# Optimization experiments

Hardware: AMD Instinct MI355X
Metric: run time of the kernel (lower is better)

The kernel has to match this reference:

```python
import jax, jax.numpy as jnp
import numpy as np

DIM = 128
H = 8
NEG_SLOPE = 0.2
SCALE = 12.0
N_ITEMS = 81920
E_INT = 163840
N_T = 4096
NUM_NODE = 40000


def _normalize(x, eps=1e-12):
    n = jnp.linalg.norm(x, axis=-1, keepdims=True)
    return x / jnp.maximum(n, eps)


def _gat(feat, src, dst, fc_w, attn_l, attn_r, bias):
    # GATConv with residual (Identity, since in_feats == out_feats) and bias.
    N = feat.shape[0]
    fs = (feat @ fc_w.T).reshape(N, H, DIM)                # [N,H,D]
    el = jnp.einsum('nhd,hd->nh', fs, attn_l)              # [N,H]
    er = jnp.einsum('nhd,hd->nh', fs, attn_r)              # [N,H]
    e = el[src] + er[dst]                                  # u_add_v -> [E,H]
    e = jnp.where(e >= 0, e, NEG_SLOPE * e)                # leaky_relu
    # edge_softmax grouped by destination node
    emax = jax.ops.segment_max(e, dst, num_segments=N)
    ex = jnp.exp(e - emax[dst])
    denom = jax.ops.segment_sum(ex, dst, num_segments=N)
    a = ex / denom[dst]                                    # [E,H]
    # u_mul_e + sum aggregation
    m = fs[src] * a[:, :, None]                            # [E,H,D]
    rst = jax.ops.segment_sum(m, dst, num_segments=N)      # [N,H,D]
    rst = rst + feat[:, None, :] + bias.reshape(1, H, DIM)
    return rst


def setup_inputs() -> dict:
    key = jax.random.key(0)
    ks = jax.random.split(key, 20)
    stdv = 1.0 / np.sqrt(DIM)

    def unif(k, shape):
        return jax.random.uniform(k, shape, jnp.float32, -stdv, stdv)

    return {
        'iid': jax.random.randint(ks[0], (N_ITEMS,), 0, NUM_NODE),
        'tid': jax.random.randint(ks[1], (N_T,), 0, 10),
        'pid': jax.random.randint(ks[2], (N_ITEMS,), 0, 200),
        'src_i': jax.random.randint(ks[3], (E_INT,), 0, N_ITEMS),
        'dst_i': jax.random.randint(ks[4], (E_INT,), 0, N_ITEMS),
        'agg_src': jnp.arange(N_ITEMS),
        'agg_dst': jnp.sort(jax.random.randint(ks[5], (N_ITEMS,), 0, N_T)),
        'last_nodes': jax.random.randint(ks[6], (N_T,), 0, N_ITEMS),
        'emb': unif(ks[7], (NUM_NODE, DIM)),
        'pos_emb': unif(ks[8], (200, DIM)),
        'target_emb': unif(ks[9], (10, DIM)),
        'gat1_fc': unif(ks[10], (H * DIM, DIM)),
        'gat1_al': unif(ks[11], (H, DIM)),
        'gat1_ar': unif(ks[12], (H, DIM)),
        'gat1_b': jnp.zeros((H * DIM,), jnp.float32),
        'gat2_fc': unif(ks[13], (H * DIM, DIM)),
        'gat2_al': unif(ks[14], (H, DIM)),
        'gat2_ar': unif(ks[15], (H, DIM)),
        'gat2_b': jnp.zeros((H * DIM,), jnp.float32),
        'q_w': unif(ks[16], (DIM, 2 * DIM)),
        'fc_sr_w': unif(ks[17], (DIM, 2 * DIM)),
    }


def reference(iid, tid, pid, src_i, dst_i, agg_src, agg_dst, last_nodes,
              emb, pos_emb, target_emb,
              gat1_fc, gat1_al, gat1_ar, gat1_b,
              gat2_fc, gat2_al, gat2_ar, gat2_b,
              q_w, fc_sr_w):
    h_v = _normalize(emb[iid])                              # [N_items, D]
    h_p = pos_emb[pid]                                      # [E_agg, D]
    h_t = target_emb[tid]                                   # [N_T, D]

    # gat1 on interacts; gat2 on reversed interacts; max over heads each
    h1 = _gat(h_v, src_i, dst_i, gat1_fc, gat1_al, gat1_ar, gat1_b).max(axis=1)
    h2 = _gat(h_v, dst_i, src_i, gat2_fc, gat2_al, gat2_ar, gat2_b).max(axis=1)
    h = _normalize(h1 + h2)                                 # [N_items, D]

    # PosAggregator over 'agg' edges (item -> target)
    ft = h[agg_src]                                         # [E_agg, D]
    e = jnp.tanh(jnp.concatenate([ft, h_p], axis=-1) @ q_w.T)
    w = jnp.sum(e * h_t[agg_dst], axis=-1, keepdims=True)   # udf_agg weight
    sr_g = jax.ops.segment_sum(ft * w, agg_dst, num_segments=h_t.shape[0])
    sr_l = h[last_nodes]                                    # last-item features

    sr = jnp.concatenate([sr_g, sr_l], axis=-1) @ fc_sr_w.T
    scores = SCALE * (_normalize(sr) @ _normalize(emb).T)   # [N_T, num_node]
    return scores
```

## Files before the change

### kernel.cpp

```cpp
#include <hip/hip_runtime.h>
#include <stdint.h>

#define DD 128
#define HN 8
#define NITEMS 81920
#define EINT 163840
#define NT 4096
#define NV 40000
#define NVPAD 40064
#define EAGG 81920
#define NEG_SLOPE 0.2f
#define SCALE 12.0f

typedef unsigned short u16;
typedef __attribute__((ext_vector_type(8))) short bf16x8;
typedef __attribute__((ext_vector_type(4))) float f32x4;
typedef __attribute__((ext_vector_type(4))) unsigned short u16x4;

__device__ __forceinline__ float bf2f(unsigned short u){ return __uint_as_float(((unsigned)u)<<16); }
__device__ __forceinline__ unsigned short f2bf(float f){
  unsigned u = __float_as_uint(f);
  u += 0x7fffu + ((u>>16)&1u);
  return (unsigned short)(u>>16);
}

__global__ __launch_bounds__(256) void k_cast3(const float* __restrict__ fc1, const float* __restrict__ fc2,
    const float* __restrict__ qw, const float* __restrict__ fcsr,
    u16* __restrict__ w1, u16* __restrict__ w2, u16* __restrict__ qb, float* __restrict__ fT){
  int i = blockIdx.x*256 + threadIdx.x;
  if (i < 131072) w1[i] = f2bf(fc1[i]);
  else if (i < 262144) w2[i-131072] = f2bf(fc2[i-131072]);
  else if (i < 294912) qb[i-262144] = f2bf(qw[i-262144]);
  else if (i < 327680){
    int j = i - 294912;
    int k = j >> 7, col = j & 127;
    fT[j] = fcsr[(size_t)col*256 + k];
  }
}

__global__ __launch_bounds__(128) void k_prep_u(const float* __restrict__ fc1, const float* __restrict__ al1,
    const float* __restrict__ ar1, const float* __restrict__ fc2, const float* __restrict__ al2,
    const float* __restrict__ ar2, u16* __restrict__ U){
  int r = blockIdx.x, k = threadIdx.x;
  if (r >= 32){ U[(size_t)r*DD + k] = 0; return; }
  int g = r>>3, h = r&7;
  const float* fc = (g>=2)? fc2 : fc1;
  const float* av = (g==0)? al1 : (g==1)? ar1 : (g==2)? al2 : ar2;
  float s = 0.f;
  for (int d=0; d<DD; ++d) s += fc[(size_t)(h*DD+d)*DD + k] * av[h*DD+d];
  U[(size_t)r*DD + k] = f2bf(s);
}

__global__ __launch_bounds__(256) void k_norm(const float* __restrict__ emb, const int* __restrict__ iid,
    u16* __restrict__ nemb, u16* __restrict__ hvb, int* __restrict__ cnt){
  int gi = blockIdx.x*256 + threadIdx.x;
  if (gi < 2*NITEMS) cnt[gi] = 0;
  int w = gi >> 6;
  int lane = gi & 63;
  u16* dst; const float* src;
  if (w < NVPAD){
    dst = nemb + (size_t)w*DD;
    if (w >= NV){ dst[lane*2]=0; dst[lane*2+1]=0; return; }
    src = emb + (size_t)w*DD;
  } else {
    int n = w - NVPAD;
    dst = hvb + (size_t)n*DD;
    src = emb + (size_t)iid[n]*DD;
  }
  float2 v = *(const float2*)(src + lane*2);
  float ss = v.x*v.x + v.y*v.y;
  #pragma unroll
  for (int m=1;m<64;m<<=1) ss += __shfl_xor(ss, m);
  float inv = 1.f / fmaxf(sqrtf(ss), 1e-12f);
  dst[lane*2]   = f2bf(v.x*inv);
  dst[lane*2+1] = f2bf(v.y*inv);
}

template<int OUT_BF16>
__global__ __launch_bounds__(256) void gemm_nt(const u16* __restrict__ A, const u16* __restrict__ B,
                                               void* __restrict__ C, int M, int N, int K,
                                               float alpha, int ldc, int nvalid){
  __shared__ u16 As[128*32];
  __shared__ u16 Bs[128*32];
  int m0 = blockIdx.x*128, n0 = blockIdx.y*128;
  int t = threadIdx.x, lane = t&63, wid = t>>6;
  int wm = wid>>1, wn = wid&1;
  f32x4 zero = {0.f,0.f,0.f,0.f};
  f32x4 acc[4][4];
  #pragma unroll
  for (int i=0;i<4;i++)
    #pragma unroll
    for (int j=0;j<4;j++) acc[i][j] = zero;
  int lr = lane & 15, lk = (lane>>4)*8;
  for (int k0=0; k0<K; k0+=32){
    #pragma unroll
    for (int cc=0; cc<2; ++cc){
      int c = t + cc*256;
      int row = c>>2, col = (c&3)*8;
      *(bf16x8*)(void*)&As[c*8] = *(const bf16x8*)(const void*)&A[(size_t)(m0+row)*K + k0 + col];
      *(bf16x8*)(void*)&Bs[c*8] = *(const bf16x8*)(const void*)&B[(size_t)(n0+row)*K + k0 + col];
    }
    __syncthreads();
    bf16x8 af[4], bfr[4];
    #pragma unroll
    for (int m=0;m<4;m++) af[m]  = *(const bf16x8*)(const void*)&As[(wm*64+m*16+lr)*32 + lk];
    #pragma unroll
    for (int n=0;n<4;n++) bfr[n] = *(const bf16x8*)(const void*)&Bs[(wn*64+n*16+lr)*32 + lk];
    #pragma unroll
    for (int m=0;m<4;m++)
      #pragma unroll
      for (int n=0;n<4;n++)
        acc[m][n] = __builtin_amdgcn_mfma_f32_16x16x32_bf16(af[m], bfr[n], acc[m][n], 0,0,0);
    __syncthreads();
  }
  #pragma unroll
  for (int m=0;m<4;m++)
    #pragma unroll
    for (int n=0;n<4;n++)
      #pragma unroll
      for (int r=0;r<4;r++){
        int row = m0 + wm*64 + m*16 + (lane>>4)*4 + r;
        int col = n0 + wn*64 + n*16 + (lane&15);
        if (col < nvalid){
          float v = acc[m][n][r]*alpha;
          if (OUT_BF16) ((u16*)C)[(size_t)row*ldc + col] = f2bf(v);
          else          ((float*)C)[(size_t)row*ldc + col] = v;
        }
      }
}

__global__ __launch_bounds__(256) void k_deg2(const int* __restrict__ di, const int* __restrict__ si,
                                              int* __restrict__ cnt){
  int i = blockIdx.x*256+threadIdx.x;
  if (i<EINT){ atomicAdd(&cnt[di[i]],1); atomicAdd(&cnt[NITEMS+si[i]],1); }
}

__global__ __launch_bounds__(256) void k_scan_a(int* cnt, int* off, int* bsum, int n){
  __shared__ int buf[256];
  int b = blockIdx.x, t = threadIdx.x, i = b*256+t;
  int v = (i<n)? cnt[i] : 0;
  buf[t] = v; __syncthreads();
  #pragma unroll
  for (int ofs=1; ofs<256; ofs<<=1){
    int x = (t>=ofs)? buf[t-ofs] : 0;
    __syncthreads();
    buf[t] += x;
    __syncthreads();
  }
  if (i<n){ off[i] = buf[t]-v; cnt[i] = 0; }
  if (t==255) bsum[b] = buf[255];
}

__global__ __launch_bounds__(1024) void k_scan_b(int* bsum, int* off, int nb, int n){
  __shared__ int buf[1024];
  int t = threadIdx.x;
  int v = (t<nb)? bsum[t] : 0;
  buf[t]=v; __syncthreads();
  #pragma unroll
  for (int ofs=1; ofs<1024; ofs<<=1){
    int x=(t>=ofs)?buf[t-ofs]:0; __syncthreads(); buf[t]+=x; __syncthreads();
  }
  if (t<nb) bsum[t] = buf[t]-v;
  if (t==1023) off[n] = buf[1023];
}

__global__ __launch_bounds__(256) void k_scan_c(int* __restrict__ off, const int* __restrict__ bsum, int n){
  int i = blockIdx.x*256+threadIdx.x;
  if (i<n) off[i] += bsum[blockIdx.x];
}

__global__ __launch_bounds__(256) void k_scatter2(const int* __restrict__ di, const int* __restrict__ si,
    const int* __restrict__ off, int* __restrict__ cnt, int* __restrict__ sid){
  int i = blockIdx.x*256+threadIdx.x;
  if (i<EINT){
    int a = di[i];         sid[off[a]+atomicAdd(&cnt[a],1)] = si[i];
    int b = NITEMS+si[i];  sid[off[b]+atomicAdd(&cnt[b],1)] = di[i];
  }
}

__global__ __launch_bounds__(256) void k_aw(const int* __restrict__ off, const int* __restrict__ sid,
    const float* __restrict__ ecat, u16* __restrict__ aw){
  int u = blockIdx.x*256 + threadIdx.x;
  if (u >= 2*NITEMS) return;
  int g = (u >= NITEMS) ? 1 : 0;
  int w = u - g*NITEMS;
  int cl = g*16, cr = g*16 + 8;
  float ern[8];
  #pragma unroll
  for (int h=0;h<8;h++) ern[h] = ecat[(size_t)w*32 + cr + h];
  int lo = off[u], hi = off[u+1];
  float den[8];
  #pragma unroll
  for (int h=0;h<8;h++) den[h] = 0.f;
  for (int i=lo;i<hi;++i){
    const float* e = ecat + (size_t)sid[i]*32 + cl;
    #pragma unroll
    for (int h=0;h<8;h++){
      float lv = e[h] + ern[h];
      lv = (lv>=0.f)? lv : NEG_SLOPE*lv;
      den[h] += expf(lv);
    }
  }
  float inv[8];
  #pragma unroll
  for (int h=0;h<8;h++) inv[h] = (den[h]>0.f)? 1.f/den[h] : 0.f;
  for (int i=lo;i<hi;++i){
    const float* e = ecat + (size_t)sid[i]*32 + cl;
    bf16x8 o;
    #pragma unroll
    for (int h=0;h<8;h++){
      float lv = e[h] + ern[h];
      lv = (lv>=0.f)? lv : NEG_SLOPE*lv;
      o[h] = (short)f2bf(expf(lv)*inv[h]);
    }
    *(bf16x8*)(void*)&aw[(size_t)i*8] = o;
  }
}

__global__ __launch_bounds__(256) void k_agg(const int* __restrict__ off, const int* __restrict__ sid,
    const u16* __restrict__ aw, const u16* __restrict__ hvb, u16* __restrict__ agg, int obase){
  int w = (blockIdx.x*256 + threadIdx.x) >> 6;
  int lane = threadIdx.x & 63;
  if (w >= NITEMS) return;
  int lo = off[obase+w], hi = off[obase+w+1];
  float a0[8], a1[8];
  #pragma unroll
  for (int h=0;h<8;h++){ a0[h]=0.f; a1[h]=0.f; }
  for (int i=lo; i<hi; ++i){
    int s = sid[i];
    unsigned v = *(const unsigned*)(const void*)&hvb[(size_t)s*DD + lane*2];
    float f0 = bf2f((u16)(v & 0xffffu)), f1 = bf2f((u16)(v >> 16));
    bf16x8 w8 = *(const bf16x8*)(const void*)&aw[(size_t)i*8];
    #pragma unroll
    for (int h=0;h<8;h++){
      float wa = bf2f((u16)w8[h]);
      a0[h] += wa*f0; a1[h] += wa*f1;
    }
  }
  #pragma unroll
  for (int h=0;h<8;h++){
    unsigned o = (unsigned)f2bf(a0[h]) | ((unsigned)f2bf(a1[h])<<16);
    *(unsigned*)(void*)&agg[(size_t)w*1024 + h*DD + lane*2] = o;
  }
}

template<int MODE>
__global__ __launch_bounds__(512) void k_hg(const u16* __restrict__ agg, const u16* __restrict__ wfc,
    const float* __restrict__ bias, const u16* __restrict__ hvb,
    u16* __restrict__ h1b, u16* __restrict__ hb){
  __shared__ __align__(16) char smem[52224];
  u16* As = (u16*)smem;
  u16* Bs = As + 64*136;
  float* F = (float*)smem;
  int n0 = blockIdx.x*64;
  int t = threadIdx.x, lane = t&63, wid = t>>6;
  int wm = wid&3, wn = wid>>2;
  int lr = lane&15, lq = lane>>4;
  int ar = t>>3, ak = (t&7)*16;
  f32x4 rm[4];
  #pragma unroll
  for (int n=0;n<4;n++){ f32x4 z={-1e30f,-1e30f,-1e30f,-1e30f}; rm[n]=z; }
  for (int h=0; h<HN; ++h){
    *(bf16x8*)(void*)&As[ar*136 + ak]     = *(const bf16x8*)(const void*)&agg[(size_t)(n0+ar)*1024 + h*DD + ak];
    *(bf16x8*)(void*)&As[ar*136 + ak + 8] = *(const bf16x8*)(const void*)&agg[(size_t)(n0+ar)*1024 + h*DD + ak + 8];
    #pragma unroll
    for (int cc=0; cc<2; ++cc){
      int c = t + cc*512;
      int br = c>>3, bk = (c&7)*16;
      *(bf16x8*)(void*)&Bs[br*136 + bk]     = *(const bf16x8*)(const void*)&wfc[(size_t)(h*DD+br)*DD + bk];
      *(bf16x8*)(void*)&Bs[br*136 + bk + 8] = *(const bf16x8*)(const void*)&wfc[(size_t)(h*DD+br)*DD + bk + 8];
    }
    __syncthreads();
    f32x4 acc[4];
    #pragma unroll
    for (int n=0;n<4;n++){ f32x4 z={0.f,0.f,0.f,0.f}; acc[n]=z; }
    #pragma unroll
    for (int ks=0; ks<4; ++ks){
      bf16x8 af = *(const bf16x8*)(const void*)&As[(wm*16+lr)*136 + ks*32 + lq*8];
      #pragma unroll
      for (int n=0;n<4;n++){
        bf16x8 bfr = *(const bf16x8*)(const void*)&Bs[(wn*64+n*16+lr)*136 + ks*32 + lq*8];
        acc[n] = __builtin_amdgcn_mfma_f32_16x16x32_bf16(af, bfr, acc[n], 0,0,0);
      }
    }
    #pragma unroll
    for (int n=0;n<4;n++){
      float bn = bias[h*DD + wn*64 + n*16 + lr];
      #pragma unroll
      for (int r=0;r<4;r++) rm[n][r] = fmaxf(rm[n][r], acc[n][r] + bn);
    }
    __syncthreads();
  }
  if (MODE==0){
    #pragma unroll
    for (int n=0;n<4;n++)
      #pragma unroll
      for (int r=0;r<4;r++){
        int row = n0 + wm*16 + lq*4 + r;
        int col = wn*64 + n*16 + lr;
        h1b[(size_t)row*DD + col] = f2bf(rm[n][r] + bf2f(hvb[(size_t)row*DD + col]));
      }
  } else {
    #pragma unroll
    for (int n=0;n<4;n++)
      #pragma unroll
      for (int r=0;r<4;r++){
        int lrow = wm*16 + lq*4 + r;
        int col = wn*64 + n*16 + lr;
        int row = n0 + lrow;
        F[lrow*DD + col] = rm[n][r] + bf2f(hvb[(size_t)row*DD + col]) + bf2f(h1b[(size_t)row*DD + col]);
      }
    __syncthreads();
    int r8 = t>>3, q = t&7;
    float vals[16];
    float ss = 0.f;
    #pragma unroll
    for (int j=0;j<16;j++){ vals[j] = F[r8*DD + q*16 + j]; ss += vals[j]*vals[j]; }
    ss += __shfl_xor(ss,1); ss += __shfl_xor(ss,2); ss += __shfl_xor(ss,4);
    float inv = 1.f/fmaxf(sqrtf(ss),1e-12f);
    bf16x8 o0, o1;
    #pragma unroll
    for (int j=0;j<8;j++){ o0[j] = (short)f2bf(vals[j]*inv); o1[j] = (short)f2bf(vals[8+j]*inv); }
    *(bf16x8*)(void*)&hb[(size_t)(n0+r8)*DD + q*16]     = o0;
    *(bf16x8*)(void*)&hb[(size_t)(n0+r8)*DD + q*16 + 8] = o1;
  }
}

__global__ __launch_bounds__(256) void k_epw(const int* __restrict__ asrc, const int* __restrict__ pid,
    const int* __restrict__ adst, const int* __restrict__ tid_, const u16* __restrict__ hb,
    const float* __restrict__ pemb, const u16* __restrict__ qwb, const float* __restrict__ temb,
    float* __restrict__ wv){
  __shared__ u16 As[128*32];
  __shared__ u16 Bs[128*32];
  __shared__ float tembS[10*DD];
  __shared__ float wsum[128];
  __shared__ int rowtt[128];
  int m0 = blockIdx.x*128;
  int t = threadIdx.x, lane = t&63, wid = t>>6;
  int wm = wid>>1, wn = wid&1, lr = lane&15, lq = lane>>4;
  for (int i=t; i<10*DD; i+=256) tembS[i] = temb[i];
  if (t < 128){ rowtt[t] = tid_[adst[m0+t]]; wsum[t] = 0.f; }
  f32x4 zero = {0.f,0.f,0.f,0.f};
  f32x4 acc[4][4];
  #pragma unroll
  for (int i=0;i<4;i++)
    #pragma unroll
    for (int j=0;j<4;j++) acc[i][j] = zero;
  for (int k0=0; k0<256; k0+=32){
    #pragma unroll
    for (int cc=0; cc<2; ++cc){
      int c = t + cc*256;
      int row = c>>2;
      int kk = k0 + (c&3)*8;
      bf16x8 av;
      if (k0 < 128){
        av = *(const bf16x8*)(const void*)&hb[(size_t)asrc[m0+row]*DD + kk];
      } else {
        const float* p = pemb + (size_t)pid[m0+row]*DD + (kk-128);
        float4 p0 = *(const float4*)p;
        float4 p1 = *(const float4*)(p+4);
        av[0]=(short)f2bf(p0.x); av[1]=(short)f2bf(p0.y); av[2]=(short)f2bf(p0.z); av[3]=(short)f2bf(p0.w);
        av[4]=(short)f2bf(p1.x); av[5]=(short)f2bf(p1.y); av[6]=(short)f2bf(p1.z); av[7]=(short)f2bf(p1.w);
      }
      *(bf16x8*)(void*)&As[c*8] = av;
      *(bf16x8*)(void*)&Bs[c*8] = *(const bf16x8*)(const void*)&qwb[(size_t)row*256 + kk];
    }
    __syncthreads();
    bf16x8 af[4], bfr[4];
    #pragma unroll
    for (int m=0;m<4;m++) af[m]  = *(const bf16x8*)(const void*)&As[(wm*64+m*16+lr)*32 + lq*8];
    #pragma unroll
    for (int n=0;n<4;n++) bfr[n] = *(const bf16x8*)(const void*)&Bs[(wn*64+n*16+lr)*32 + lq*8];
    #pragma unroll
    for (int m=0;m<4;m++)
      #pragma unroll
      for (int n=0;n<4;n++)
        acc[m][n] = __builtin_amdgcn_mfma_f32_16x16x32_bf16(af[m], bfr[n], acc[m][n], 0,0,0);
    __syncthreads();
  }
  #pragma unroll
  for (int m=0;m<4;m++)
    #pragma unroll
    for (int r=0;r<4;r++){
      int lrow = wm*64 + m*16 + lq*4 + r;
      int tt = rowtt[lrow];
      float p = 0.f;
      #pragma unroll
      for (int n=0;n<4;n++){
        int col = wn*64 + n*16 + lr;
        p += tanhf(acc[m][n][r]) * tembS[tt*DD + col];
      }
      #pragma unroll
      for (int msk=1; msk<16; msk<<=1) p += __shfl_xor(p, msk);
      if (lr==0) atomicAdd(&wsum[lrow], p);
    }
  __syncthreads();
  if (t < 128) wv[m0+t] = wsum[t];
}

__device__ __forceinline__ int lbound(const int* a, int n, int key){
  int lo=0, hi=n;
  while (lo<hi){ int mid=(lo+hi)>>1; if (a[mid]<key) lo=mid+1; else hi=mid; }
  return lo;
}

__global__ __launch_bounds__(256) void k_sr(const u16* __restrict__ hb, const float* __restrict__ w,
    const int* __restrict__ asrc, const int* __restrict__ adst, const int* __restrict__ lastn,
    const float* __restrict__ fcsrT, u16* __restrict__ nsr){
  __shared__ float cat[256];
  __shared__ float red[128];
  __shared__ int lohi[2];
  int t = blockIdx.x, tid = threadIdx.x;
  if (tid == 0){ lohi[0] = lbound(adst, EAGG, t); lohi[1] = lbound(adst, EAGG, t+1); }
  __syncthreads();
  int lo = lohi[0], hi = lohi[1];
  if (tid < DD){
    float a = 0.f;
    for (int i=lo;i<hi;++i) a += bf2f(hb[(size_t)asrc[i]*DD + tid]) * w[i];
    cat[tid] = a;
  } else {
    int d = tid - DD;
    cat[DD + d] = bf2f(hb[(size_t)lastn[t]*DD + d]);
  }
  __syncthreads();
  float s = 0.f;
  if (tid < DD){
    #pragma unroll 8
    for (int k=0;k<256;++k) s += cat[k]*fcsrT[(size_t)k*DD + tid];
    red[tid] = s*s;
  }
  __syncthreads();
  for (int st=64; st>0; st>>=1){
    if (tid < st) red[tid] += red[tid+st];
    __syncthreads();
  }
  if (tid < DD){
    float inv = 1.f/fmaxf(sqrtf(red[0]),1e-12f);
    nsr[(size_t)t*DD + tid] = f2bf(s*inv);
  }
}

__global__ __launch_bounds__(256) void gemm_sc(const u16* __restrict__ A, const u16* __restrict__ B,
                                               float* __restrict__ C){
  __shared__ __align__(16) char smem[16896];
  u16* As = (u16*)smem;
  u16* Bs = As + 4096;
  float* tr = (float*)smem;
  int flat = blockIdx.y*gridDim.x + blockIdx.x;
  int nf = (flat&7)*1252 + (flat>>3);
  int m0 = (nf & 31)*128;
  int n0 = (nf >> 5)*128;
  int t = threadIdx.x, lane = t&63, wid = t>>6;
  int wm = wid>>1, wn = wid&1, lr = lane&15, lq = lane>>4;
  f32x4 zero = {0.f,0.f,0.f,0.f};
  f32x4 acc[4][4];
  #pragma unroll
  for (int i=0;i<4;i++)
    #pragma unroll
    for (int j=0;j<4;j++) acc[i][j] = zero;
  for (int k0=0; k0<DD; k0+=32){
    #pragma unroll
    for (int cc=0; cc<2; ++cc){
      int c = t + cc*256;
      int row = c>>2, col = (c&3)*8;
      *(bf16x8*)(void*)&As[c*8] = *(const bf16x8*)(const void*)&A[(size_t)(m0+row)*DD + k0 + col];
      *(bf16x8*)(void*)&Bs[c*8] = *(const bf16x8*)(const void*)&B[(size_t)(n0+row)*DD + k0 + col];
    }
    __syncthreads();
    bf16x8 af[4], bfr[4];
    #pragma unroll
    for (int m=0;m<4;m++) af[m]  = *(const bf16x8*)(const void*)&As[(wm*64+m*16+lr)*32 + lq*8];
    #pragma unroll
    for (int n=0;n<4;n++) bfr[n] = *(const bf16x8*)(const void*)&Bs[(wn*64+n*16+lr)*32 + lq*8];
    #pragma unroll
    for (int m=0;m<4;m++)
      #pragma unroll
      for (int n=0;n<4;n++)
        acc[m][n] = __builtin_amdgcn_mfma_f32_16x16x32_bf16(af[m], bfr[n], acc[m][n], 0,0,0);
    __syncthreads();
  }
  int rr = lane>>4;
  int cq = lane&15;
  #pragma unroll
  for (int m=0;m<4;m++){
    #pragma unroll
    for (int n=0;n<4;n++)
      #pragma unroll
      for (int r=0;r<4;r++)
        tr[wid*1040 + (lq*4+r)*65 + n*16 + lr] = acc[m][n][r]*SCALE;
    __syncthreads();
    #pragma unroll
    for (int rg=0; rg<4; ++rg){
      int row = rg*4 + rr;
      int grow = m0 + wm*64 + m*16 + row;
      int gcol = n0 + wn*64 + cq*4;
      if (gcol < NV)
        *(float4*)&C[(size_t)grow*NV + gcol] = *(const float4*)&tr[wid*1040 + row*65 + cq*4];
    }
    __syncthreads();
  }
}

extern "C" void kernel_launch(void* const* d_in, const int* in_sizes, int n_in,
                              void* d_out, int out_size, void* d_ws, size_t ws_size,
                              hipStream_t stream){
  (void)in_sizes; (void)n_in; (void)out_size; (void)ws_size;
  const int*   iid   = (const int*)d_in[0];
  const int*   tid_  = (const int*)d_in[1];
  const int*   pid   = (const int*)d_in[2];
  const int*   src_i = (const int*)d_in[3];
  const int*   dst_i = (const int*)d_in[4];
  const int*   asrc  = (const int*)d_in[5];
  const int*   adst  = (const int*)d_in[6];
  const int*   lastn = (const int*)d_in[7];
  const float* emb   = (const float*)d_in[8];
  const float* pemb  = (const float*)d_in[9];
  const float* temb  = (const float*)d_in[10];
  const float* fc1   = (const float*)d_in[11];
  const float* al1   = (const float*)d_in[12];
  const float* ar1   = (const float*)d_in[13];
  const float* b1    = (const float*)d_in[14];
  const float* fc2   = (const float*)d_in[15];
  const float* al2   = (const float*)d_in[16];
  const float* ar2   = (const float*)d_in[17];
  const float* b2    = (const float*)d_in[18];
  const float* qw    = (const float*)d_in[19];
  const float* fcsr  = (const float*)d_in[20];

  char* ws = (char*)d_ws;
  size_t o = 0;
  auto alc = [&](size_t b)->char*{ char* r = ws + o; o += (b + 511) & ~(size_t)511; return r; };
  u16*   hvb  = (u16*)  alc((size_t)NITEMS*DD*2);
  u16*   hb   = (u16*)  alc((size_t)NITEMS*DD*2);
  u16*   h1b  = (u16*)  alc((size_t)NITEMS*DD*2);
  float* ecat = (float*)alc((size_t)NITEMS*32*4);
  int*   off  = (int*)  alc((size_t)(2*NITEMS+1)*4);
  int*   cnt  = (int*)  alc((size_t)(2*NITEMS)*4);
  int*   bsum = (int*)  alc((size_t)1024*4);
  int*   sid  = (int*)  alc((size_t)(2*EINT)*4);
  u16*   aw   = (u16*)  alc((size_t)(2*EINT)*8*2);
  u16*   wfc1 = (u16*)  alc((size_t)1024*DD*2);
  u16*   wfc2 = (u16*)  alc((size_t)1024*DD*2);
  u16*   qwb  = (u16*)  alc((size_t)DD*256*2);
  float* fT   = (float*)alc((size_t)256*DD*4);
  u16*   Umat = (u16*)  alc((size_t)128*DD*2);
  float* wv   = (float*)alc((size_t)EAGG*4);
  u16*   nsr  = (u16*)  alc((size_t)NT*DD*2);
  u16*   nemb = (u16*)  alc((size_t)NVPAD*DD*2);
  u16*   agg  = (u16*)  alc((size_t)NITEMS*1024*2);

  const int N2 = 2*NITEMS;
  const int NB2 = N2/256;

  k_norm<<<(NVPAD+NITEMS)/4, 256, 0, stream>>>(emb, iid, nemb, hvb, cnt);
  k_prep_u<<<128, 128, 0, stream>>>(fc1, al1, ar1, fc2, al2, ar2, Umat);
  k_cast3<<<1280, 256, 0, stream>>>(fc1, fc2, qw, fcsr, wfc1, wfc2, qwb, fT);
  gemm_nt<0><<<dim3(NITEMS/128, 1), 256, 0, stream>>>(hvb, Umat, ecat, NITEMS, 128, DD, 1.f, 32, 32);

  k_deg2<<<(EINT+255)/256, 256, 0, stream>>>(dst_i, src_i, cnt);
  k_scan_a<<<NB2, 256, 0, stream>>>(cnt, off, bsum, N2);
  k_scan_b<<<1, 1024, 0, stream>>>(bsum, off, NB2, N2);
  k_scan_c<<<NB2, 256, 0, stream>>>(off, bsum, N2);
  k_scatter2<<<(EINT+255)/256, 256, 0, stream>>>(dst_i, src_i, off, cnt, sid);

  k_aw<<<N2/256, 256, 0, stream>>>(off, sid, ecat, aw);

  k_agg<<<NITEMS/4, 256, 0, stream>>>(off, sid, aw, hvb, agg, 0);
  k_hg<0><<<NITEMS/64, 512, 0, stream>>>(agg, wfc1, b1, hvb, h1b, nullptr);
  k_agg<<<NITEMS/4, 256, 0, stream>>>(off, sid, aw, hvb, agg, NITEMS);
  k_hg<1><<<NITEMS/64, 512, 0, stream>>>(agg, wfc2, b2, hvb, h1b, hb);

  k_epw<<<EAGG/128, 256, 0, stream>>>(asrc, pid, adst, tid_, hb, pemb, qwb, temb, wv);
  k_sr<<<NT, 256, 0, stream>>>(hb, wv, asrc, adst, lastn, fT, nsr);

  gemm_sc<<<dim3(32, NVPAD/128), 256, 0, stream>>>(nsr, nemb, (float*)d_out);
}
```

Measured before the change: 554.6 us.

## Merge prep kernels, fold scan fixup into consumers, retile score GEMM

The three setup kernels (normalize, attention-vector projection, weight casts) become one launch with block ranges. The final scan-add kernel is removed: consumers add the per-block sum when they read offsets, and the scan writes a zero sentinel for the last block. The score GEMM moves to 64x256 tiles with a K step of 64, padded LDS rows and a 1D swizzled grid, with NVPAD raised to a multiple of 256. This cuts launch overhead and aims for better reuse and stores in the dominant output GEMM, at the cost of extra offset reads and more LDS per block.

```diff
diff --git a/kernel.cpp b/kernel.cpp
--- a/kernel.cpp
+++ b/kernel.cpp
@@ -7,10 +7,14 @@
 #define EINT 163840
 #define NT 4096
 #define NV 40000
-#define NVPAD 40064
+#define NVPAD 40192
 #define EAGG 81920
 #define NEG_SLOPE 0.2f
 #define SCALE 12.0f
+
+#define NB_NORM ((NVPAD + NITEMS)/4)
+#define NB_PU 64
+#define NB_CAST 1280
 
 typedef unsigned short u16;
 typedef __attribute__((ext_vector_type(8))) short bf16x8;
@@ -24,56 +28,56 @@
   return (unsigned short)(u>>16);
 }
 
-__global__ __launch_bounds__(256) void k_cast3(const float* __restrict__ fc1, const float* __restrict__ fc2,
+__global__ __launch_bounds__(256) void k_prep(const float* __restrict__ emb, const int* __restrict__ iid,
+    const float* __restrict__ fc1, const float* __restrict__ al1, const float* __restrict__ ar1,
+    const float* __restrict__ fc2, const float* __restrict__ al2, const float* __restrict__ ar2,
     const float* __restrict__ qw, const float* __restrict__ fcsr,
+    u16* __restrict__ nemb, u16* __restrict__ hvb, int* __restrict__ cnt, u16* __restrict__ U,
     u16* __restrict__ w1, u16* __restrict__ w2, u16* __restrict__ qb, float* __restrict__ fT){
-  int i = blockIdx.x*256 + threadIdx.x;
-  if (i < 131072) w1[i] = f2bf(fc1[i]);
-  else if (i < 262144) w2[i-131072] = f2bf(fc2[i-131072]);
-  else if (i < 294912) qb[i-262144] = f2bf(qw[i-262144]);
-  else if (i < 327680){
-    int j = i - 294912;
-    int k = j >> 7, col = j & 127;
-    fT[j] = fcsr[(size_t)col*256 + k];
-  }
-}
-
-__global__ __launch_bounds__(128) void k_prep_u(const float* __restrict__ fc1, const float* __restrict__ al1,
-    const float* __restrict__ ar1, const float* __restrict__ fc2, const float* __restrict__ al2,
-    const float* __restrict__ ar2, u16* __restrict__ U){
-  int r = blockIdx.x, k = threadIdx.x;
-  if (r >= 32){ U[(size_t)r*DD + k] = 0; return; }
-  int g = r>>3, h = r&7;
-  const float* fc = (g>=2)? fc2 : fc1;
-  const float* av = (g==0)? al1 : (g==1)? ar1 : (g==2)? al2 : ar2;
-  float s = 0.f;
-  for (int d=0; d<DD; ++d) s += fc[(size_t)(h*DD+d)*DD + k] * av[h*DD+d];
-  U[(size_t)r*DD + k] = f2bf(s);
-}
-
-__global__ __launch_bounds__(256) void k_norm(const float* __restrict__ emb, const int* __restrict__ iid,
-    u16* __restrict__ nemb, u16* __restrict__ hvb, int* __restrict__ cnt){
-  int gi = blockIdx.x*256 + threadIdx.x;
-  if (gi < 2*NITEMS) cnt[gi] = 0;
-  int w = gi >> 6;
-  int lane = gi & 63;
-  u16* dst; const float* src;
-  if (w < NVPAD){
-    dst = nemb + (size_t)w*DD;
-    if (w >= NV){ dst[lane*2]=0; dst[lane*2+1]=0; return; }
-    src = emb + (size_t)w*DD;
+  int b = blockIdx.x;
+  if (b < NB_NORM){
+    int gi = b*256 + threadIdx.x;
+    if (gi < 2*NITEMS) cnt[gi] = 0;
+    int w = gi >> 6;
+    int lane = gi & 63;
+    u16* dst; const float* src;
+    if (w < NVPAD){
+      dst = nemb + (size_t)w*DD;
+      if (w >= NV){ dst[lane*2]=0; dst[lane*2+1]=0; return; }
+      src = emb + (size_t)w*DD;
+    } else {
+      int n = w - NVPAD;
+      dst = hvb + (size_t)n*DD;
+      src = emb + (size_t)iid[n]*DD;
+    }
+    float2 v = *(const float2*)(src + lane*2);
+    float ss = v.x*v.x + v.y*v.y;
+    #pragma unroll
+    for (int m=1;m<64;m<<=1) ss += __shfl_xor(ss, m);
+    float inv = 1.f / fmaxf(sqrtf(ss), 1e-12f);
+    dst[lane*2]   = f2bf(v.x*inv);
+    dst[lane*2+1] = f2bf(v.y*inv);
+  } else if (b < NB_NORM + NB_PU){
+    int r = (b - NB_NORM)*2 + (threadIdx.x>>7);
+    int k = threadIdx.x & 127;
+    if (r >= 32){ U[(size_t)r*DD + k] = 0; return; }
+    int g = r>>3, h = r&7;
+    const float* fc = (g>=2)? fc2 : fc1;
+    const float* av = (g==0)? al1 : (g==1)? ar1 : (g==2)? al2 : ar2;
+    float s = 0.f;
+    for (int d=0; d<DD; ++d) s += fc[(size_t)(h*DD+d)*DD + k] * av[h*DD+d];
+    U[(size_t)r*DD + k] = f2bf(s);
   } else {
-    int n = w - NVPAD;
-    dst = hvb + (size_t)n*DD;
-    src = emb + (size_t)iid[n]*DD;
-  }
-  float2 v = *(const float2*)(src + lane*2);
-  float ss = v.x*v.x + v.y*v.y;
-  #pragma unroll
-  for (int m=1;m<64;m<<=1) ss += __shfl_xor(ss, m);
-  float inv = 1.f / fmaxf(sqrtf(ss), 1e-12f);
-  dst[lane*2]   = f2bf(v.x*inv);
-  dst[lane*2+1] = f2bf(v.y*inv);
+    int i = (b - NB_NORM - NB_PU)*256 + threadIdx.x;
+    if (i < 131072) w1[i] = f2bf(fc1[i]);
+    else if (i < 262144) w2[i-131072] = f2bf(fc2[i-131072]);
+    else if (i < 294912) qb[i-262144] = f2bf(qw[i-262144]);
+    else if (i < 327680){
+      int j = i - 294912;
+      int k = j >> 7, col = j & 127;
+      fT[j] = fcsr[(size_t)col*256 + k];
+    }
+  }
 }
 
 template<int OUT_BF16>
@@ -161,25 +165,21 @@
     int x=(t>=ofs)?buf[t-ofs]:0; __syncthreads(); buf[t]+=x; __syncthreads();
   }
   if (t<nb) bsum[t] = buf[t]-v;
+  else if (t==nb) bsum[t] = 0;
   if (t==1023) off[n] = buf[1023];
 }
 
-__global__ __launch_bounds__(256) void k_scan_c(int* __restrict__ off, const int* __restrict__ bsum, int n){
-  int i = blockIdx.x*256+threadIdx.x;
-  if (i<n) off[i] += bsum[blockIdx.x];
-}
-
 __global__ __launch_bounds__(256) void k_scatter2(const int* __restrict__ di, const int* __restrict__ si,
-    const int* __restrict__ off, int* __restrict__ cnt, int* __restrict__ sid){
+    const int* __restrict__ off, const int* __restrict__ bsum, int* __restrict__ cnt, int* __restrict__ sid){
   int i = blockIdx.x*256+threadIdx.x;
   if (i<EINT){
-    int a = di[i];         sid[off[a]+atomicAdd(&cnt[a],1)] = si[i];
-    int b = NITEMS+si[i];  sid[off[b]+atomicAdd(&cnt[b],1)] = di[i];
-  }
-}
-
-__global__ __launch_bounds__(256) void k_aw(const int* __restrict__ off, const int* __restrict__ sid,
-    const float* __restrict__ ecat, u16* __restrict__ aw){
+    int a = di[i];         sid[off[a]+bsum[a>>8]+atomicAdd(&cnt[a],1)] = si[i];
+    int b = NITEMS+si[i];  sid[off[b]+bsum[b>>8]+atomicAdd(&cnt[b],1)] = di[i];
+  }
+}
+
+__global__ __launch_bounds__(256) void k_aw(const int* __restrict__ off, const int* __restrict__ bsum,
+    const int* __restrict__ sid, const float* __restrict__ ecat, u16* __restrict__ aw){
   int u = blockIdx.x*256 + threadIdx.x;
   if (u >= 2*NITEMS) return;
   int g = (u >= NITEMS) ? 1 : 0;
@@ -188,7 +188,8 @@
   float ern[8];
   #pragma unroll
   for (int h=0;h<8;h++) ern[h] = ecat[(size_t)w*32 + cr + h];
-  int lo = off[u], hi = off[u+1];
+  int lo = off[u] + bsum[u>>8];
+  int hi = off[u+1] + bsum[(u+1)>>8];
   float den[8];
   #pragma unroll
   for (int h=0;h<8;h++) den[h] = 0.f;
@@ -217,12 +218,15 @@
   }
 }
 
-__global__ __launch_bounds__(256) void k_agg(const int* __restrict__ off, const int* __restrict__ sid,
-    const u16* __restrict__ aw, const u16* __restrict__ hvb, u16* __restrict__ agg, int obase){
+__global__ __launch_bounds__(256) void k_agg(const int* __restrict__ off, const int* __restrict__ bsum,
+    const int* __restrict__ sid, const u16* __restrict__ aw, const u16* __restrict__ hvb,
+    u16* __restrict__ agg, int obase){
   int w = (blockIdx.x*256 + threadIdx.x) >> 6;
   int lane = threadIdx.x & 63;
   if (w >= NITEMS) return;
-  int lo = off[obase+w], hi = off[obase+w+1];
+  int u = obase + w;
+  int lo = off[u] + bsum[u>>8];
+  int hi = off[u+1] + bsum[(u+1)>>8];
   float a0[8], a1[8];
   #pragma unroll
   for (int h=0;h<8;h++){ a0[h]=0.f; a1[h]=0.f; }
@@ -442,45 +446,52 @@
 
 __global__ __launch_bounds__(256) void gemm_sc(const u16* __restrict__ A, const u16* __restrict__ B,
                                                float* __restrict__ C){
-  __shared__ __align__(16) char smem[16896];
+  __shared__ __align__(16) char smem[46080];
   u16* As = (u16*)smem;
-  u16* Bs = As + 4096;
+  u16* Bs = As + 64*72;
   float* tr = (float*)smem;
-  int flat = blockIdx.y*gridDim.x + blockIdx.x;
-  int nf = (flat&7)*1252 + (flat>>3);
-  int m0 = (nf & 31)*128;
-  int n0 = (nf >> 5)*128;
+  int flat = blockIdx.x;
+  int nf = (flat&7)*1256 + (flat>>3);
+  int nti = nf % 157, mti = nf / 157;
+  int m0 = mti*64, n0 = nti*256;
   int t = threadIdx.x, lane = t&63, wid = t>>6;
-  int wm = wid>>1, wn = wid&1, lr = lane&15, lq = lane>>4;
+  int lr = lane&15, lq = lane>>4;
   f32x4 zero = {0.f,0.f,0.f,0.f};
   f32x4 acc[4][4];
   #pragma unroll
   for (int i=0;i<4;i++)
     #pragma unroll
     for (int j=0;j<4;j++) acc[i][j] = zero;
-  for (int k0=0; k0<DD; k0+=32){
-    #pragma unroll
-    for (int cc=0; cc<2; ++cc){
-      int c = t + cc*256;
-      int row = c>>2, col = (c&3)*8;
-      *(bf16x8*)(void*)&As[c*8] = *(const bf16x8*)(const void*)&A[(size_t)(m0+row)*DD + k0 + col];
-      *(bf16x8*)(void*)&Bs[c*8] = *(const bf16x8*)(const void*)&B[(size_t)(n0+row)*DD + k0 + col];
-    }
-    __syncthreads();
-    bf16x8 af[4], bfr[4];
-    #pragma unroll
-    for (int m=0;m<4;m++) af[m]  = *(const bf16x8*)(const void*)&As[(wm*64+m*16+lr)*32 + lq*8];
-    #pragma unroll
-    for (int n=0;n<4;n++) bfr[n] = *(const bf16x8*)(const void*)&Bs[(wn*64+n*16+lr)*32 + lq*8];
-    #pragma unroll
-    for (int m=0;m<4;m++)
-      #pragma unroll
-      for (int n=0;n<4;n++)
-        acc[m][n] = __builtin_amdgcn_mfma_f32_16x16x32_bf16(af[m], bfr[n], acc[m][n], 0,0,0);
-    __syncthreads();
-  }
-  int rr = lane>>4;
-  int cq = lane&15;
+  for (int k0=0; k0<DD; k0+=64){
+    #pragma unroll
+    for (int i=0;i<2;++i){
+      int c = t + i*256;
+      int row = c>>3, kk = (c&7)*8;
+      *(bf16x8*)(void*)&As[row*72 + kk] = *(const bf16x8*)(const void*)&A[(size_t)(m0+row)*DD + k0 + kk];
+    }
+    #pragma unroll
+    for (int i=0;i<8;++i){
+      int c = t + i*256;
+      int row = c>>3, kk = (c&7)*8;
+      *(bf16x8*)(void*)&Bs[row*72 + kk] = *(const bf16x8*)(const void*)&B[(size_t)(n0+row)*DD + k0 + kk];
+    }
+    __syncthreads();
+    #pragma unroll
+    for (int ks=0; ks<2; ++ks){
+      bf16x8 af[4], bfr[4];
+      #pragma unroll
+      for (int m=0;m<4;m++) af[m]  = *(const bf16x8*)(const void*)&As[(m*16+lr)*72 + ks*32 + lq*8];
+      #pragma unroll
+      for (int n=0;n<4;n++) bfr[n] = *(const bf16x8*)(const void*)&Bs[(wid*64+n*16+lr)*72 + ks*32 + lq*8];
+      #pragma unroll
+      for (int m=0;m<4;m++)
+        #pragma unroll
+        for (int n=0;n<4;n++)
+          acc[m][n] = __builtin_amdgcn_mfma_f32_16x16x32_bf16(af[m], bfr[n], acc[m][n], 0,0,0);
+    }
+    __syncthreads();
+  }
+  int rr = lane>>4, cq = lane&15;
   #pragma unroll
   for (int m=0;m<4;m++){
     #pragma unroll
@@ -492,8 +503,8 @@
     #pragma unroll
     for (int rg=0; rg<4; ++rg){
       int row = rg*4 + rr;
-      int grow = m0 + wm*64 + m*16 + row;
-      int gcol = n0 + wn*64 + cq*4;
+      int grow = m0 + m*16 + row;
+      int gcol = n0 + wid*64 + cq*4;
       if (gcol < NV)
         *(float4*)&C[(size_t)grow*NV + gcol] = *(const float4*)&tr[wid*1040 + row*65 + cq*4];
     }
@@ -552,26 +563,24 @@
   const int N2 = 2*NITEMS;
   const int NB2 = N2/256;
 
-  k_norm<<<(NVPAD+NITEMS)/4, 256, 0, stream>>>(emb, iid, nemb, hvb, cnt);
-  k_prep_u<<<128, 128, 0, stream>>>(fc1, al1, ar1, fc2, al2, ar2, Umat);
-  k_cast3<<<1280, 256, 0, stream>>>(fc1, fc2, qw, fcsr, wfc1, wfc2, qwb, fT);
+  k_prep<<<NB_NORM + NB_PU + NB_CAST, 256, 0, stream>>>(emb, iid, fc1, al1, ar1, fc2, al2, ar2,
+      qw, fcsr, nemb, hvb, cnt, Umat, wfc1, wfc2, qwb, fT);
   gemm_nt<0><<<dim3(NITEMS/128, 1), 256, 0, stream>>>(hvb, Umat, ecat, NITEMS, 128, DD, 1.f, 32, 32);
 
   k_deg2<<<(EINT+255)/256, 256, 0, stream>>>(dst_i, src_i, cnt);
   k_scan_a<<<NB2, 256, 0, stream>>>(cnt, off, bsum, N2);
   k_scan_b<<<1, 1024, 0, stream>>>(bsum, off, NB2, N2);
-  k_scan_c<<<NB2, 256, 0, stream>>>(off, bsum, N2);
-  k_scatter2<<<(EINT+255)/256, 256, 0, stream>>>(dst_i, src_i, off, cnt, sid);
-
-  k_aw<<<N2/256, 256, 0, stream>>>(off, sid, ecat, aw);
-
-  k_agg<<<NITEMS/4, 256, 0, stream>>>(off, sid, aw, hvb, agg, 0);
+  k_scatter2<<<(EINT+255)/256, 256, 0, stream>>>(dst_i, src_i, off, bsum, cnt, sid);
+
+  k_aw<<<N2/256, 256, 0, stream>>>(off, bsum, sid, ecat, aw);
+
+  k_agg<<<NITEMS/4, 256, 0, stream>>>(off, bsum, sid, aw, hvb, agg, 0);
   k_hg<0><<<NITEMS/64, 512, 0, stream>>>(agg, wfc1, b1, hvb, h1b, nullptr);
-  k_agg<<<NITEMS/4, 256, 0, stream>>>(off, sid, aw, hvb, agg, NITEMS);
+  k_agg<<<NITEMS/4, 256, 0, stream>>>(off, bsum, sid, aw, hvb, agg, NITEMS);
   k_hg<1><<<NITEMS/64, 512, 0, stream>>>(agg, wfc2, b2, hvb, h1b, hb);
 
   k_epw<<<EAGG/128, 256, 0, stream>>>(asrc, pid, adst, tid_, hb, pemb, qwb, temb, wv);
   k_sr<<<NT, 256, 0, stream>>>(hb, wv, asrc, adst, lastn, fT, nsr);
 
-  gemm_sc<<<dim3(32, NVPAD/128), 256, 0, stream>>>(nsr, nemb, (float*)d_out);
-}
+  gemm_sc<<<10048, 256, 0, stream>>>(nsr, nemb, (float*)d_out);
+}
```

New measurement: 559.7 us. No clear change (+0.9%).
